# Kernel optimization log

Measured on AMD Instinct MI355X. Metric: run time of the kernel, lower is better.

## Reference

```python
import jax, jax.numpy as jnp
import numpy as np

B, C, H, W = 2, 192, 96, 96
HEADS, DG, KH, KW = 12, 12, 3, 3
K = KH * KW
PAD, DIL = KH // 2, 1
MLP_HIDDEN = 2 * C  # mlp_ratio = 2


def setup_inputs() -> dict:
    key = jax.random.key(0)
    ks = jax.random.split(key, 14)
    s = 0.02
    return {
        "q": jax.random.normal(ks[0], (B, C, H, W), jnp.float32),
        "k": jax.random.normal(ks[1], (B, C, H, W), jnp.float32),
        "v": jax.random.normal(ks[2], (B, C, H, W), jnp.float32),
        "offset": jax.random.normal(ks[3], (B, DG * 2 * K, H, W), jnp.float32),
        "Wq": jax.random.normal(ks[4], (C, C), jnp.float32) * s,
        "bq": jax.random.normal(ks[5], (C,), jnp.float32) * s,
        "Wk": jax.random.normal(ks[6], (C, C), jnp.float32) * s,
        "bk": jax.random.normal(ks[7], (C,), jnp.float32) * s,
        "Wv": jax.random.normal(ks[8], (C, C), jnp.float32) * s,
        "bv": jax.random.normal(ks[9], (C,), jnp.float32) * s,
        "W1": jax.random.normal(ks[10], (C, MLP_HIDDEN), jnp.float32) * s,
        "b1": jax.random.normal(ks[11], (MLP_HIDDEN,), jnp.float32) * s,
        "W2": jax.random.normal(ks[12], (MLP_HIDDEN, C), jnp.float32) * s,
        "b2": jax.random.normal(ks[13], (C,), jnp.float32) * s,
    }


def _bilinear_sample(img, py, px):
    """img: [B,G,Cg,H,W]; py,px: [B,G,K,H,W] fractional sample coords.
    Returns [B,G,Cg,K,H,W]; zero outside image (DCN-style per-corner masking)."""
    b, g, cg, h, w = img.shape
    y0 = jnp.floor(py)
    x0 = jnp.floor(px)
    wy1 = py - y0
    wx1 = px - x0
    wy0 = 1.0 - wy1
    wx0 = 1.0 - wx1
    imgf = img.reshape(b, g, cg, h * w)

    def corner(yi, xi, wgt):
        valid = ((yi >= 0) & (yi <= h - 1) & (xi >= 0) & (xi <= w - 1)).astype(img.dtype)
        yc = jnp.clip(yi, 0, h - 1).astype(jnp.int32)
        xc = jnp.clip(xi, 0, w - 1).astype(jnp.int32)
        idx = (yc * w + xc).reshape(b, g, 1, -1)  # [B,G,1,K*H*W]
        gth = jnp.take_along_axis(imgf, idx, axis=3)  # [B,G,Cg,K*H*W]
        return gth * (valid * wgt).reshape(b, g, 1, -1)

    out = (corner(y0, x0, wy0 * wx0)
           + corner(y0, x0 + 1, wy0 * wx1)
           + corner(y0 + 1, x0, wy1 * wx0)
           + corner(y0 + 1, x0 + 1, wy1 * wx1))
    return out.reshape(b, g, cg, py.shape[2], h, w)


def _forward(q, k, v, offset, Wq, bq, Wk, bk, Wv, bv, W1, b1, W2, b2):
    def lin(x, Wm, bb):  # per-pixel Linear over channel dim
        return jnp.einsum('bchw,cd->bdhw', x, Wm) + bb[None, :, None, None]

    qp = lin(q, Wq, bq)
    kp = lin(k, Wk, bk)
    vp = lin(v, Wv, bv)

    # DCN-v1 offset layout: [B, G, K, 2(y,x), H, W]
    off = offset.reshape(B, DG, K, 2, H, W)
    ii, jj = jnp.meshgrid(jnp.arange(KH), jnp.arange(KW), indexing='ij')
    ii = ii.reshape(K)
    jj = jj.reshape(K)
    base_y = (jnp.arange(H)[None, :] - PAD + (ii * DIL)[:, None]).astype(jnp.float32)  # [K,H]
    base_x = (jnp.arange(W)[None, :] - PAD + (jj * DIL)[:, None]).astype(jnp.float32)  # [K,W]
    py = base_y[None, None, :, :, None] + off[:, :, :, 0]  # [B,G,K,H,W]
    px = base_x[None, None, :, None, :] + off[:, :, :, 1]

    cg = C // DG
    k_s = _bilinear_sample(kp.reshape(B, DG, cg, H, W), py, px)  # [B,G,cg,K,H,W]
    v_s = _bilinear_sample(vp.reshape(B, DG, cg, H, W), py, px)

    hd = C // HEADS
    k_s = k_s.reshape(B, HEADS, hd, K, H, W)
    v_s = v_s.reshape(B, HEADS, hd, K, H, W)
    qh = qp.reshape(B, HEADS, hd, H, W)

    scale = hd ** -0.5
    scores = jnp.einsum('bndhw,bndkhw->bnkhw', qh, k_s) * scale
    attn = jax.nn.softmax(scores, axis=2)  # over K sampled points (clip_size=1)
    out = jnp.einsum('bnkhw,bndkhw->bndhw', attn, v_s).reshape(B, C, H, W)

    # residual MLP (GELU exact, as torch nn.GELU default)
    xf = out.transpose(0, 2, 3, 1)  # [B,H,W,C]
    h1 = jax.nn.gelu(xf @ W1 + b1, approximate=False)
    mlp = (h1 @ W2 + b2).transpose(0, 3, 1, 2)
    return out + mlp


def reference(q, k, v, offset, Wq, bq, Wk, bk, Wv, bv, W1, b1, W2, b2):
    return _forward(q, k, v, offset, Wq, bq, Wk, bk, Wv, bv, W1, b1, W2, b2)
```

## Files before the change

### kernel.cpp

```cpp
#include <hip/hip_runtime.h>
#include <hip/hip_bf16.h>
#include <math.h>

#define B_    2
#define C_    192
#define H_    96
#define W_    96
#define HW_   (H_ * W_)
#define NPIX_ (B_ * HW_)
#define G_    12
#define CG_   16
#define KPTS_ 9
#define MLPH_ 384

typedef __attribute__((ext_vector_type(8))) short s16x8;
typedef __attribute__((ext_vector_type(4))) float f32x4;

__device__ __forceinline__ ushort f2b(float f) {
    __hip_bfloat16 h = __float2bfloat16(f);
    return *reinterpret_cast<ushort*>(&h);
}
__device__ __forceinline__ float b2f(ushort u) {
    return __uint_as_float(((uint)u) << 16);
}
__device__ __forceinline__ float b2f_lo(uint u) { return __uint_as_float(u << 16); }
__device__ __forceinline__ float b2f_hi(uint u) { return __uint_as_float(u & 0xffff0000u); }

#define GLOAD16(gp, lp)                                                          \
    __builtin_amdgcn_global_load_lds(                                            \
        (const __attribute__((address_space(1))) void*)(gp),                     \
        (__attribute__((address_space(3))) void*)(lp), 16, 0, 0)

__global__ __launch_bounds__(256) void pack_kernel(
    const float* __restrict__ q, const float* __restrict__ k,
    const float* __restrict__ v, ushort* __restrict__ Xcl)
{
    __shared__ ushort sm[64][200];
    const int t   = threadIdx.x;
    const int hw0 = blockIdx.x * 64;
    const int b   = blockIdx.y;
    const int z   = blockIdx.z;
    const float* X = (z == 0) ? q : (z == 1) ? k : v;

    const int hwl = t & 63;
    #pragma unroll 4
    for (int j = 0; j < 48; ++j) {
        const int c = (t >> 6) + j * 4;
        sm[hwl][c] = f2b(X[(b * C_ + c) * HW_ + hw0 + hwl]);
    }
    __syncthreads();
    #pragma unroll
    for (int jj = 0; jj < 6; ++jj) {
        const int idx = t + 256 * jj;
        const int row = idx / 24, cq = idx - row * 24;
        const int pix = b * HW_ + hw0 + row;
        *(uint4*)&Xcl[((z * NPIX_) + pix) * C_ + cq * 8] = *(uint4*)&sm[row][cq * 8];
    }
}

__global__ __launch_bounds__(256) void wpack_kernel(
    const float* __restrict__ Wq, const float* __restrict__ Wk,
    const float* __restrict__ Wv, const float* __restrict__ W1,
    const float* __restrict__ W2, ushort* __restrict__ Wt)
{
    const int i = blockIdx.x * 256 + threadIdx.x;
    if (i < 110592) {
        const int s = i / 36864, j = i - s * 36864;
        const float* src = (s == 0) ? Wq : (s == 1) ? Wk : Wv;
        const int d = j / 192, c = j - d * 192;
        Wt[i] = f2b(src[c * 192 + d]);
    } else if (i < 184320) {
        const int j = i - 110592, d = j / 192, c = j - d * 192;
        Wt[i] = f2b(W1[c * 384 + d]);
    } else if (i < 258048) {
        const int j = i - 184320, d = j / 384, c = j - d * 384;
        Wt[i] = f2b(W2[c * 192 + d]);
    }
}

template<int KK>
__device__ __forceinline__ void stage_tiles(const ushort* Az, const ushort* Bz,
                                            ushort* dst, int t, int m0, int n0, int kt)
{
    const int r0 = t >> 2, s0 = t & 3;
    const int c0 = s0 ^ ((r0 >> 1) & 3);
    const int r1 = r0 + 64;
    const int c1 = s0 ^ ((r1 >> 1) & 3);
    GLOAD16(Az + (m0 + r0) * KK + kt * 32 + c0 * 8, dst + t * 8);
    GLOAD16(Az + (m0 + r1) * KK + kt * 32 + c1 * 8, dst + 2048 + t * 8);
    GLOAD16(Bz + (n0 + r0) * KK + kt * 32 + c0 * 8, dst + 4096 + t * 8);
}

template<int KK, int EPI>
__global__ __launch_bounds__(256) void gemm_kernel(
    const ushort* __restrict__ A,  const ushort* __restrict__ BT,
    const float* __restrict__ bias0, const float* __restrict__ bias1,
    const float* __restrict__ bias2,
    ushort* __restrict__ Ob,
    const ushort* __restrict__ res, float* __restrict__ Onchw,
    int zAstr, int zBstr, int zOstr)
{
    constexpr int LDS_SZ = (EPI == 2) ? (64 * 132 * 4) : 24576;
    __shared__ char lds_raw[LDS_SZ < 24576 ? 24576 : LDS_SZ];
    ushort* smem = (ushort*)lds_raw;

    const int t  = threadIdx.x;
    const int l  = t & 63;
    const int wid = t >> 6;
    const int wm = wid >> 1, wn = wid & 1;
    const int m0 = blockIdx.x * 128;
    const int n0 = blockIdx.y * 64;
    const int z  = blockIdx.z;
    const int Ntot = gridDim.y * 64;
    constexpr int NKT = KK / 32;

    const ushort* Az = A  + (size_t)z * zAstr;
    const ushort* Bz = BT + (size_t)z * zBstr;
    const float* bias = (z == 0) ? bias0 : (z == 1) ? bias1 : bias2;

    int aoff[4], boff[2];
    #pragma unroll
    for (int f = 0; f < 4; ++f) {
        const int r = wm * 64 + f * 16 + (l & 15);
        const int s = (l >> 4) ^ ((r >> 1) & 3);
        aoff[f] = r * 32 + s * 8;
    }
    #pragma unroll
    for (int g = 0; g < 2; ++g) {
        const int r = wn * 32 + g * 16 + (l & 15);
        const int s = (l >> 4) ^ ((r >> 1) & 3);
        boff[g] = 4096 + r * 32 + s * 8;
    }

    f32x4 acc[4][2] = {};

    stage_tiles<KK>(Az, Bz, smem, t, m0, n0, 0);
    __syncthreads();

    for (int kt = 0; kt < NKT; ++kt) {
        const int cur = kt & 1;
        if (kt + 1 < NKT)
            stage_tiles<KK>(Az, Bz, smem + ((kt + 1) & 1) * 6144, t, m0, n0, kt + 1);

        const ushort* buf = smem + cur * 6144;
        s16x8 af[4], bf[2];
        #pragma unroll
        for (int f = 0; f < 4; ++f) af[f] = *(const s16x8*)(buf + aoff[f]);
        #pragma unroll
        for (int g = 0; g < 2; ++g) bf[g] = *(const s16x8*)(buf + boff[g]);
        #pragma unroll
        for (int f = 0; f < 4; ++f)
            #pragma unroll
            for (int g = 0; g < 2; ++g)
                acc[f][g] = __builtin_amdgcn_mfma_f32_16x16x32_bf16(af[f], bf[g], acc[f][g], 0, 0, 0);
        __syncthreads();
    }

    const int rowg = l >> 4, ncol = l & 15;
    float bv[2];
    #pragma unroll
    for (int g = 0; g < 2; ++g) bv[g] = bias[n0 + wn * 32 + g * 16 + ncol];

    if (EPI == 0) {
        ushort* O = Ob + (size_t)z * zOstr;
        #pragma unroll
        for (int f = 0; f < 4; ++f)
            #pragma unroll
            for (int g = 0; g < 2; ++g)
                #pragma unroll
                for (int r = 0; r < 4; ++r) {
                    const int m = m0 + wm * 64 + f * 16 + rowg * 4 + r;
                    const int n = n0 + wn * 32 + g * 16 + ncol;
                    O[(size_t)m * Ntot + n] = f2b(acc[f][g][r] + bv[g]);
                }
    } else if (EPI == 1) {
        #pragma unroll
        for (int f = 0; f < 4; ++f)
            #pragma unroll
            for (int g = 0; g < 2; ++g)
                #pragma unroll
                for (int r = 0; r < 4; ++r) {
                    const int m = m0 + wm * 64 + f * 16 + rowg * 4 + r;
                    const int n = n0 + wn * 32 + g * 16 + ncol;
                    const float x = acc[f][g][r] + bv[g];
                    Ob[(size_t)m * Ntot + n] = f2b(0.5f * x * (1.f + erff(x * 0.70710678118f)));
                }
    } else {
        float* tsp = (float*)lds_raw;
        #pragma unroll
        for (int f = 0; f < 4; ++f)
            #pragma unroll
            for (int g = 0; g < 2; ++g)
                #pragma unroll
                for (int r = 0; r < 4; ++r) {
                    const int ml = wm * 64 + f * 16 + rowg * 4 + r;
                    const int nl = wn * 32 + g * 16 + ncol;
                    const float rv = b2f(res[(size_t)(m0 + ml) * C_ + n0 + nl]);
                    tsp[nl * 132 + ml] = acc[f][g][r] + bv[g] + rv;
                }
        __syncthreads();
        const int b   = m0 / HW_;
        const int hw0 = m0 - b * HW_;
        #pragma unroll
        for (int jj = 0; jj < 8; ++jj) {
            const int i4 = t + 256 * jj;
            const int nn = i4 >> 5, mc = i4 & 31;
            float4 val = *(float4*)&tsp[nn * 132 + mc * 4];
            *(float4*)&Onchw[(size_t)b * C_ * HW_ + (size_t)(n0 + nn) * HW_ + hw0 + mc * 4] = val;
        }
    }
}

__global__ __launch_bounds__(256, 4) void deform_attn_kernel(
    const ushort* __restrict__ qp, const ushort* __restrict__ kp,
    const ushort* __restrict__ vp, const float* __restrict__ offset,
    ushort* __restrict__ aob)
{
    const int t   = threadIdx.x;
    const int bid = blockIdx.x;
    const int xb  = (bid & 7) * 432 + (bid >> 3);
    const int pair = xb * 64 + (t >> 2);
    const int lane4 = t & 3;
    const int g   = pair % G_;
    const int pix = pair / G_;
    const int b   = pix / HW_;
    const int hw  = pix - b * HW_;
    const int h   = hw / W_;
    const int w   = hw - h * W_;
    const int gc0 = g * CG_ + lane4 * 4;

    float q0, q1, q2, q3;
    {
        uint2 qu = *(const uint2*)(qp + pix * C_ + gc0);
        q0 = b2f_lo(qu.x); q1 = b2f_hi(qu.x);
        q2 = b2f_lo(qu.y); q3 = b2f_hi(qu.y);
    }

    float offy[3] = {0.f, 0.f, 0.f}, offx[3] = {0.f, 0.f, 0.f};
    {
        const int obase = (b * (G_ * 2 * KPTS_) + g * (2 * KPTS_)) * HW_ + hw;
        #pragma unroll
        for (int s = 0; s < 3; ++s) {
            const int kk = lane4 + s * 4;
            if (kk < KPTS_) {
                offy[s] = offset[obase + (kk * 2) * HW_];
                offx[s] = offset[obase + (kk * 2 + 1) * HW_];
            }
        }
    }

    const ushort* kp_b = kp + (size_t)b * HW_ * C_;
    const ushort* vp_b = vp + (size_t)b * HW_ * C_;

    float score[KPTS_];
    f32x4 vsamp[KPTS_];

    #pragma unroll
    for (int kk = 0; kk < KPTS_; ++kk) {
        const float oy = __shfl(offy[kk >> 2], kk & 3, 4);
        const float ox = __shfl(offx[kk >> 2], kk & 3, 4);
        const float py = (float)(h - 1 + kk / 3) + oy;
        const float px = (float)(w - 1 + kk % 3) + ox;
        const float fy = floorf(py), fx = floorf(px);
        const int   y0 = (int)fy,   x0 = (int)fx;
        const float wy1 = py - fy, wx1 = px - fx;
        const float wy0 = 1.f - wy1, wx0 = 1.f - wx1;

        f32x4 ks = {0.f, 0.f, 0.f, 0.f};
        f32x4 vs = {0.f, 0.f, 0.f, 0.f};
        #define CORNER(yy, xx, wgt)                                               \
            if ((unsigned)(yy) < (unsigned)H_ && (unsigned)(xx) < (unsigned)W_) { \
                const int a = ((yy) * W_ + (xx)) * C_ + gc0;                      \
                const uint2 ku = *(const uint2*)(kp_b + a);                       \
                const uint2 vu = *(const uint2*)(vp_b + a);                       \
                const float wg = (wgt);                                           \
                ks[0] = fmaf(wg, b2f_lo(ku.x), ks[0]);                            \
                ks[1] = fmaf(wg, b2f_hi(ku.x), ks[1]);                            \
                ks[2] = fmaf(wg, b2f_lo(ku.y), ks[2]);                            \
                ks[3] = fmaf(wg, b2f_hi(ku.y), ks[3]);                            \
                vs[0] = fmaf(wg, b2f_lo(vu.x), vs[0]);                            \
                vs[1] = fmaf(wg, b2f_hi(vu.x), vs[1]);                            \
                vs[2] = fmaf(wg, b2f_lo(vu.y), vs[2]);                            \
                vs[3] = fmaf(wg, b2f_hi(vu.y), vs[3]);                            \
            }
        CORNER(y0,     x0,     wy0 * wx0)
        CORNER(y0,     x0 + 1, wy0 * wx1)
        CORNER(y0 + 1, x0,     wy1 * wx0)
        CORNER(y0 + 1, x0 + 1, wy1 * wx1)
        #undef CORNER

        float sc = q0 * ks[0];
        sc = fmaf(q1, ks[1], sc);
        sc = fmaf(q2, ks[2], sc);
        sc = fmaf(q3, ks[3], sc);
        sc += __shfl_xor(sc, 1, 4);
        sc += __shfl_xor(sc, 2, 4);
        score[kk] = sc * 0.25f;
        vsamp[kk] = vs;
    }

    float m = score[0];
    #pragma unroll
    for (int kk = 1; kk < KPTS_; ++kk) m = fmaxf(m, score[kk]);
    float s = 0.f;
    #pragma unroll
    for (int kk = 0; kk < KPTS_; ++kk) { score[kk] = __expf(score[kk] - m); s += score[kk]; }
    const float inv = 1.f / s;

    f32x4 o = {0.f, 0.f, 0.f, 0.f};
    #pragma unroll
    for (int kk = 0; kk < KPTS_; ++kk) {
        o[0] = fmaf(score[kk], vsamp[kk][0], o[0]);
        o[1] = fmaf(score[kk], vsamp[kk][1], o[1]);
        o[2] = fmaf(score[kk], vsamp[kk][2], o[2]);
        o[3] = fmaf(score[kk], vsamp[kk][3], o[3]);
    }

    uint2 ob;
    ob.x = (uint)f2b(o[0] * inv) | ((uint)f2b(o[1] * inv) << 16);
    ob.y = (uint)f2b(o[2] * inv) | ((uint)f2b(o[3] * inv) << 16);
    *(uint2*)(aob + pix * C_ + gc0) = ob;
}

extern "C" void kernel_launch(void* const* d_in, const int* in_sizes, int n_in,
                              void* d_out, int out_size, void* d_ws, size_t ws_size,
                              hipStream_t stream)
{
    const float* q      = (const float*)d_in[0];
    const float* k      = (const float*)d_in[1];
    const float* v      = (const float*)d_in[2];
    const float* offset = (const float*)d_in[3];
    const float* Wq     = (const float*)d_in[4];
    const float* bq     = (const float*)d_in[5];
    const float* Wk     = (const float*)d_in[6];
    const float* bk     = (const float*)d_in[7];
    const float* Wv     = (const float*)d_in[8];
    const float* bv     = (const float*)d_in[9];
    const float* W1     = (const float*)d_in[10];
    const float* b1     = (const float*)d_in[11];
    const float* W2     = (const float*)d_in[12];
    const float* b2     = (const float*)d_in[13];

    ushort* Xcl = (ushort*)d_ws;
    ushort* aob = Xcl;
    ushort* qkv = Xcl + 3 * NPIX_ * C_;
    ushort* Hb  = qkv + 3 * NPIX_ * C_;
    ushort* Wt  = Hb + (size_t)NPIX_ * MLPH_;
    ushort* W1T = Wt + 110592;
    ushort* W2T = Wt + 184320;

    pack_kernel<<<dim3(HW_ / 64, B_, 3), 256, 0, stream>>>(q, k, v, Xcl);
    wpack_kernel<<<1008, 256, 0, stream>>>(Wq, Wk, Wv, W1, W2, Wt);

    gemm_kernel<192, 0><<<dim3(NPIX_ / 128, 3, 3), 256, 0, stream>>>(
        Xcl, Wt, bq, bk, bv, qkv, nullptr, nullptr,
        NPIX_ * C_, C_ * C_, NPIX_ * C_);

    deform_attn_kernel<<<NPIX_ * G_ / 64, 256, 0, stream>>>(
        qkv, qkv + NPIX_ * C_, qkv + 2 * NPIX_ * C_, offset, aob);

    gemm_kernel<192, 1><<<dim3(NPIX_ / 128, 6, 1), 256, 0, stream>>>(
        aob, W1T, b1, b1, b1, Hb, nullptr, nullptr, 0, 0, 0);

    gemm_kernel<384, 2><<<dim3(NPIX_ / 128, 3, 1), 256, 0, stream>>>(
        Hb, W2T, b2, b2, b2, nullptr, aob, (float*)d_out, 0, 0, 0);
}
```

Measured before the change: 216.4 us.

## Deepen GEMM K-tile, restructure deform sampling into two passes, narrow pack stores

The GEMM now stages 64-wide K tiles with an 8-way XOR swizzle, which halves the number of loop iterations and barriers per tile at the cost of doubling LDS to 48KB. The deformable attention kernel precomputes clamped corner addresses and masked weights for all 9 points. It then gathers K in one pass for the scores and V in a second pass after the softmax, so the per-point V samples no longer need to be held in registers. Occupancy is lowered to 2 blocks per SM to make room for the address and weight arrays. The pack kernel switches to 8-byte stores with a smaller LDS row pitch.

```diff
diff --git a/kernel.cpp b/kernel.cpp
--- a/kernel.cpp
+++ b/kernel.cpp
@@ -35,7 +35,7 @@
     const float* __restrict__ q, const float* __restrict__ k,
     const float* __restrict__ v, ushort* __restrict__ Xcl)
 {
-    __shared__ ushort sm[64][200];
+    __shared__ ushort sm[64][196];
     const int t   = threadIdx.x;
     const int hw0 = blockIdx.x * 64;
     const int b   = blockIdx.y;
@@ -50,11 +50,11 @@
     }
     __syncthreads();
     #pragma unroll
-    for (int jj = 0; jj < 6; ++jj) {
+    for (int jj = 0; jj < 12; ++jj) {
         const int idx = t + 256 * jj;
-        const int row = idx / 24, cq = idx - row * 24;
+        const int row = idx / 48, cq = idx - row * 48;
         const int pix = b * HW_ + hw0 + row;
-        *(uint4*)&Xcl[((z * NPIX_) + pix) * C_ + cq * 8] = *(uint4*)&sm[row][cq * 8];
+        *(uint2*)&Xcl[((z * NPIX_) + pix) * C_ + cq * 4] = *(uint2*)&sm[row][cq * 4];
     }
 }
 
@@ -79,16 +79,23 @@
 }
 
 template<int KK>
-__device__ __forceinline__ void stage_tiles(const ushort* Az, const ushort* Bz,
-                                            ushort* dst, int t, int m0, int n0, int kt)
-{
-    const int r0 = t >> 2, s0 = t & 3;
-    const int c0 = s0 ^ ((r0 >> 1) & 3);
-    const int r1 = r0 + 64;
-    const int c1 = s0 ^ ((r1 >> 1) & 3);
-    GLOAD16(Az + (m0 + r0) * KK + kt * 32 + c0 * 8, dst + t * 8);
-    GLOAD16(Az + (m0 + r1) * KK + kt * 32 + c1 * 8, dst + 2048 + t * 8);
-    GLOAD16(Bz + (n0 + r0) * KK + kt * 32 + c0 * 8, dst + 4096 + t * 8);
+__device__ __forceinline__ void stage_tiles64(const ushort* Az, const ushort* Bz,
+                                              ushort* dst, int t, int m0, int n0, int kt)
+{
+    #pragma unroll
+    for (int j = 0; j < 4; ++j) {
+        const int q = t + 256 * j;
+        const int r = q >> 3, p = q & 7;
+        const int s = p ^ (r & 7);
+        GLOAD16(Az + (size_t)(m0 + r) * KK + kt * 64 + s * 8, dst + q * 8);
+    }
+    #pragma unroll
+    for (int j = 0; j < 2; ++j) {
+        const int q = t + 256 * j;
+        const int r = q >> 3, p = q & 7;
+        const int s = p ^ (r & 7);
+        GLOAD16(Bz + (size_t)(n0 + r) * KK + kt * 64 + s * 8, dst + 8192 + q * 8);
+    }
 }
 
 template<int KK, int EPI>
@@ -100,8 +107,7 @@
     const ushort* __restrict__ res, float* __restrict__ Onchw,
     int zAstr, int zBstr, int zOstr)
 {
-    constexpr int LDS_SZ = (EPI == 2) ? (64 * 132 * 4) : 24576;
-    __shared__ char lds_raw[LDS_SZ < 24576 ? 24576 : LDS_SZ];
+    __shared__ char lds_raw[49152];
     ushort* smem = (ushort*)lds_raw;
 
     const int t  = threadIdx.x;
@@ -112,47 +118,58 @@
     const int n0 = blockIdx.y * 64;
     const int z  = blockIdx.z;
     const int Ntot = gridDim.y * 64;
-    constexpr int NKT = KK / 32;
+    constexpr int NKT = KK / 64;
 
     const ushort* Az = A  + (size_t)z * zAstr;
     const ushort* Bz = BT + (size_t)z * zBstr;
     const float* bias = (z == 0) ? bias0 : (z == 1) ? bias1 : bias2;
 
-    int aoff[4], boff[2];
+    int aoff[4][2], boff[2][2];
     #pragma unroll
     for (int f = 0; f < 4; ++f) {
         const int r = wm * 64 + f * 16 + (l & 15);
-        const int s = (l >> 4) ^ ((r >> 1) & 3);
-        aoff[f] = r * 32 + s * 8;
+        #pragma unroll
+        for (int ks = 0; ks < 2; ++ks) {
+            const int c = ks * 4 + (l >> 4);
+            aoff[f][ks] = r * 64 + (c ^ (r & 7)) * 8;
+        }
     }
     #pragma unroll
     for (int g = 0; g < 2; ++g) {
         const int r = wn * 32 + g * 16 + (l & 15);
-        const int s = (l >> 4) ^ ((r >> 1) & 3);
-        boff[g] = 4096 + r * 32 + s * 8;
+        #pragma unroll
+        for (int ks = 0; ks < 2; ++ks) {
+            const int c = ks * 4 + (l >> 4);
+            boff[g][ks] = 8192 + r * 64 + (c ^ (r & 7)) * 8;
+        }
     }
 
     f32x4 acc[4][2] = {};
 
-    stage_tiles<KK>(Az, Bz, smem, t, m0, n0, 0);
+    stage_tiles64<KK>(Az, Bz, smem, t, m0, n0, 0);
     __syncthreads();
 
     for (int kt = 0; kt < NKT; ++kt) {
-        const int cur = kt & 1;
         if (kt + 1 < NKT)
-            stage_tiles<KK>(Az, Bz, smem + ((kt + 1) & 1) * 6144, t, m0, n0, kt + 1);
-
-        const ushort* buf = smem + cur * 6144;
-        s16x8 af[4], bf[2];
-        #pragma unroll
-        for (int f = 0; f < 4; ++f) af[f] = *(const s16x8*)(buf + aoff[f]);
-        #pragma unroll
-        for (int g = 0; g < 2; ++g) bf[g] = *(const s16x8*)(buf + boff[g]);
+            stage_tiles64<KK>(Az, Bz, smem + ((kt + 1) & 1) * 12288, t, m0, n0, kt + 1);
+
+        const ushort* buf = smem + (kt & 1) * 12288;
+        s16x8 af[4][2], bf[2][2];
         #pragma unroll
         for (int f = 0; f < 4; ++f)
             #pragma unroll
-            for (int g = 0; g < 2; ++g)
-                acc[f][g] = __builtin_amdgcn_mfma_f32_16x16x32_bf16(af[f], bf[g], acc[f][g], 0, 0, 0);
+            for (int ks = 0; ks < 2; ++ks) af[f][ks] = *(const s16x8*)(buf + aoff[f][ks]);
+        #pragma unroll
+        for (int g = 0; g < 2; ++g)
+            #pragma unroll
+            for (int ks = 0; ks < 2; ++ks) bf[g][ks] = *(const s16x8*)(buf + boff[g][ks]);
+        #pragma unroll
+        for (int ks = 0; ks < 2; ++ks)
+            #pragma unroll
+            for (int f = 0; f < 4; ++f)
+                #pragma unroll
+                for (int g = 0; g < 2; ++g)
+                    acc[f][g] = __builtin_amdgcn_mfma_f32_16x16x32_bf16(af[f][ks], bf[g][ks], acc[f][g], 0, 0, 0);
         __syncthreads();
     }
 
@@ -211,7 +228,7 @@
     }
 }
 
-__global__ __launch_bounds__(256, 4) void deform_attn_kernel(
+__global__ __launch_bounds__(256, 2) void deform_attn_kernel(
     const ushort* __restrict__ qp, const ushort* __restrict__ kp,
     const ushort* __restrict__ vp, const float* __restrict__ offset,
     ushort* __restrict__ aob)
@@ -249,12 +266,8 @@
         }
     }
 
-    const ushort* kp_b = kp + (size_t)b * HW_ * C_;
-    const ushort* vp_b = vp + (size_t)b * HW_ * C_;
-
-    float score[KPTS_];
-    f32x4 vsamp[KPTS_];
-
+    int   addr[KPTS_][4];
+    float wgt[KPTS_][4];
     #pragma unroll
     for (int kk = 0; kk < KPTS_; ++kk) {
         const float oy = __shfl(offy[kk >> 2], kk & 3, 4);
@@ -266,59 +279,73 @@
         const float wy1 = py - fy, wx1 = px - fx;
         const float wy0 = 1.f - wy1, wx0 = 1.f - wx1;
 
-        f32x4 ks = {0.f, 0.f, 0.f, 0.f};
-        f32x4 vs = {0.f, 0.f, 0.f, 0.f};
-        #define CORNER(yy, xx, wgt)                                               \
-            if ((unsigned)(yy) < (unsigned)H_ && (unsigned)(xx) < (unsigned)W_) { \
-                const int a = ((yy) * W_ + (xx)) * C_ + gc0;                      \
-                const uint2 ku = *(const uint2*)(kp_b + a);                       \
-                const uint2 vu = *(const uint2*)(vp_b + a);                       \
-                const float wg = (wgt);                                           \
-                ks[0] = fmaf(wg, b2f_lo(ku.x), ks[0]);                            \
-                ks[1] = fmaf(wg, b2f_hi(ku.x), ks[1]);                            \
-                ks[2] = fmaf(wg, b2f_lo(ku.y), ks[2]);                            \
-                ks[3] = fmaf(wg, b2f_hi(ku.y), ks[3]);                            \
-                vs[0] = fmaf(wg, b2f_lo(vu.x), vs[0]);                            \
-                vs[1] = fmaf(wg, b2f_hi(vu.x), vs[1]);                            \
-                vs[2] = fmaf(wg, b2f_lo(vu.y), vs[2]);                            \
-                vs[3] = fmaf(wg, b2f_hi(vu.y), vs[3]);                            \
-            }
-        CORNER(y0,     x0,     wy0 * wx0)
-        CORNER(y0,     x0 + 1, wy0 * wx1)
-        CORNER(y0 + 1, x0,     wy1 * wx0)
-        CORNER(y0 + 1, x0 + 1, wy1 * wx1)
-        #undef CORNER
-
-        float sc = q0 * ks[0];
-        sc = fmaf(q1, ks[1], sc);
-        sc = fmaf(q2, ks[2], sc);
-        sc = fmaf(q3, ks[3], sc);
+        const float wy0m = ((unsigned)y0       < (unsigned)H_) ? wy0 : 0.f;
+        const float wy1m = ((unsigned)(y0 + 1) < (unsigned)H_) ? wy1 : 0.f;
+        const float wx0m = ((unsigned)x0       < (unsigned)W_) ? wx0 : 0.f;
+        const float wx1m = ((unsigned)(x0 + 1) < (unsigned)W_) ? wx1 : 0.f;
+        const int yc0 = min(max(y0, 0), H_ - 1);
+        const int yc1 = min(max(y0 + 1, 0), H_ - 1);
+        const int xc0 = min(max(x0, 0), W_ - 1);
+        const int xc1 = min(max(x0 + 1, 0), W_ - 1);
+
+        addr[kk][0] = (yc0 * W_ + xc0) * C_ + gc0;  wgt[kk][0] = wy0m * wx0m;
+        addr[kk][1] = (yc0 * W_ + xc1) * C_ + gc0;  wgt[kk][1] = wy0m * wx1m;
+        addr[kk][2] = (yc1 * W_ + xc0) * C_ + gc0;  wgt[kk][2] = wy1m * wx0m;
+        addr[kk][3] = (yc1 * W_ + xc1) * C_ + gc0;  wgt[kk][3] = wy1m * wx1m;
+    }
+
+    const ushort* kp_b = kp + (size_t)b * HW_ * C_;
+    const ushort* vp_b = vp + (size_t)b * HW_ * C_;
+
+    float score[KPTS_];
+    #pragma unroll
+    for (int kk = 0; kk < KPTS_; ++kk) {
+        float s = 0.f;
+        #pragma unroll
+        for (int c = 0; c < 4; ++c) {
+            const uint2 ku = *(const uint2*)(kp_b + addr[kk][c]);
+            float d = q0 * b2f_lo(ku.x);
+            d = fmaf(q1, b2f_hi(ku.x), d);
+            d = fmaf(q2, b2f_lo(ku.y), d);
+            d = fmaf(q3, b2f_hi(ku.y), d);
+            s = fmaf(wgt[kk][c], d, s);
+        }
+        score[kk] = s;
+    }
+    #pragma unroll
+    for (int kk = 0; kk < KPTS_; ++kk) {
+        float sc = score[kk];
         sc += __shfl_xor(sc, 1, 4);
         sc += __shfl_xor(sc, 2, 4);
         score[kk] = sc * 0.25f;
-        vsamp[kk] = vs;
     }
 
     float m = score[0];
     #pragma unroll
     for (int kk = 1; kk < KPTS_; ++kk) m = fmaxf(m, score[kk]);
-    float s = 0.f;
-    #pragma unroll
-    for (int kk = 0; kk < KPTS_; ++kk) { score[kk] = __expf(score[kk] - m); s += score[kk]; }
-    const float inv = 1.f / s;
+    float ssum = 0.f;
+    #pragma unroll
+    for (int kk = 0; kk < KPTS_; ++kk) { score[kk] = __expf(score[kk] - m); ssum += score[kk]; }
+    const float inv = 1.f / ssum;
 
     f32x4 o = {0.f, 0.f, 0.f, 0.f};
     #pragma unroll
     for (int kk = 0; kk < KPTS_; ++kk) {
-        o[0] = fmaf(score[kk], vsamp[kk][0], o[0]);
-        o[1] = fmaf(score[kk], vsamp[kk][1], o[1]);
-        o[2] = fmaf(score[kk], vsamp[kk][2], o[2]);
-        o[3] = fmaf(score[kk], vsamp[kk][3], o[3]);
+        const float p = score[kk] * inv;
+        #pragma unroll
+        for (int c = 0; c < 4; ++c) {
+            const float pw = p * wgt[kk][c];
+            const uint2 vu = *(const uint2*)(vp_b + addr[kk][c]);
+            o[0] = fmaf(pw, b2f_lo(vu.x), o[0]);
+            o[1] = fmaf(pw, b2f_hi(vu.x), o[1]);
+            o[2] = fmaf(pw, b2f_lo(vu.y), o[2]);
+            o[3] = fmaf(pw, b2f_hi(vu.y), o[3]);
+        }
     }
 
     uint2 ob;
-    ob.x = (uint)f2b(o[0] * inv) | ((uint)f2b(o[1] * inv) << 16);
-    ob.y = (uint)f2b(o[2] * inv) | ((uint)f2b(o[3] * inv) << 16);
+    ob.x = (uint)f2b(o[0]) | ((uint)f2b(o[1]) << 16);
+    ob.y = (uint)f2b(o[2]) | ((uint)f2b(o[3]) << 16);
     *(uint2*)(aob + pix * C_ + gc0) = ob;
 }
 
```

Measured after the change: 200.7 us. 7.3% less time.
